# Kernel tuning notes

Measured on AMD Instinct MI355X. Metric: run time of the kernel, lower is better.

## Reference

```python
import jax, jax.numpy as jnp
import numpy as np

D_MODEL = 1024
N_HEAD = 16
D_HEAD = D_MODEL // N_HEAD
B, S = 4, 2048


def setup_inputs() -> dict:
    key = jax.random.key(0)
    ks = jax.random.split(key, 9)
    s = 1.0 / np.sqrt(D_MODEL)
    inp = {"x": jax.random.normal(ks[0], (B, S, D_MODEL), dtype=jnp.float32)}
    for i, name in enumerate(["q", "k", "v", "o"]):
        inp[f"W{name}"] = jax.random.uniform(ks[1 + 2 * i], (D_MODEL, D_MODEL), jnp.float32, -s, s)
        inp[f"b{name}"] = jax.random.uniform(ks[2 + 2 * i], (D_MODEL,), jnp.float32, -s, s)
    return inp


def reference(x, Wq, bq, Wk, bk, Wv, bv, Wo, bo):
    b, sq, _ = x.shape
    skv = sq
    # projections (torch Linear: x @ W^T + b), reshape to (b, h, s, d)
    def proj(W, bias):
        return (x @ W.T + bias).reshape(b, sq, N_HEAD, D_HEAD).transpose(0, 2, 1, 3)
    q, k, v = proj(Wq, bq), proj(Wk, bk), proj(Wv, bv)
    scale = np.sqrt(D_HEAD).astype(np.float32)
    scores = jnp.einsum("bhqd,bhkd->bhqk", q, k) / scale
    causal_mask = jnp.triu(jnp.ones((sq, skv), dtype=bool), k=1)
    scores = jnp.where(causal_mask, -jnp.inf, scores)
    attn = jax.nn.softmax(scores, axis=-1)
    o = jnp.einsum("bhqk,bhkd->bhqd", attn, v)  # (b, h, sq, d_head)
    o = o.transpose(0, 2, 1, 3).reshape(b, sq, D_MODEL)
    return o @ Wo.T + bo
```

## Files before the change

kernel.cpp:

```cpp
#include <hip/hip_runtime.h>
#include <hip/hip_bf16.h>
#include <math.h>

#define S_LEN 2048
#define DMODEL 1024
#define NHEAD 16
#define DHEAD 64
#define BATCH 4
#define MROWS (BATCH * S_LEN)

typedef unsigned short u16;
typedef __attribute__((ext_vector_type(4))) unsigned short u16x4;
typedef __attribute__((ext_vector_type(8))) unsigned short u16x8;
typedef __attribute__((ext_vector_type(2))) unsigned u32x2;
typedef __attribute__((ext_vector_type(4))) unsigned u32x4;
typedef __attribute__((ext_vector_type(8))) short bf16x8;
typedef __attribute__((ext_vector_type(4))) float f32x4;

__device__ __forceinline__ u16 f2bf(float f) {
  unsigned u = __float_as_uint(f);
  u += 0x7fff + ((u >> 16) & 1);
  return (u16)(u >> 16);
}

__device__ __forceinline__ unsigned pkbf2(float lo, float hi) {
  __hip_bfloat162 h = __float22bfloat162_rn(float2{lo, hi});
  unsigned r;
  __builtin_memcpy(&r, &h, 4);
  return r;
}

__device__ __forceinline__ float exp2v(float x) {
  float r;
  asm("v_exp_f32 %0, %1" : "=v"(r) : "v"(x));
  return r;
}

__device__ __forceinline__ f32x4 mfma16(bf16x8 a, bf16x8 b, f32x4 c) {
  return __builtin_amdgcn_mfma_f32_16x16x32_bf16(a, b, c, 0, 0, 0);
}

__global__ __launch_bounds__(256) void castall(
    const float* __restrict__ x,
    const float* __restrict__ w0, const float* __restrict__ w1,
    const float* __restrict__ w2, const float* __restrict__ w3,
    u16* __restrict__ ox,
    u16* __restrict__ o0, u16* __restrict__ o1,
    u16* __restrict__ o2, u16* __restrict__ o3) {
  const int blk = blockIdx.x;
  const float* in;
  u16* out;
  int base;
  if (blk < 4096)      { in = x;  out = ox; base = blk; }
  else if (blk < 4608) { in = w0; out = o0; base = blk - 4096; }
  else if (blk < 5120) { in = w1; out = o1; base = blk - 4608; }
  else if (blk < 5632) { in = w2; out = o2; base = blk - 5120; }
  else                 { in = w3; out = o3; base = blk - 5632; }
  const int i = (base * 256 + threadIdx.x) * 8;
  f32x4 v0 = *(const f32x4*)(in + i);
  f32x4 v1 = *(const f32x4*)(in + i + 4);
  u16x8 o;
#pragma unroll
  for (int j = 0; j < 4; ++j) { o[j] = f2bf(v0[j]); o[4 + j] = f2bf(v1[j]); }
  *(u16x8*)(out + i) = o;
}

__global__ __launch_bounds__(256) void gemm_qkv(
    const u16* __restrict__ Xb,
    const u16* __restrict__ W0, const u16* __restrict__ W1, const u16* __restrict__ W2,
    const float* __restrict__ b0, const float* __restrict__ b1, const float* __restrict__ b2,
    u16* __restrict__ O0, u16* __restrict__ O1, u16* __restrict__ O2) {
  __shared__ u16 As[128 * 64];
  __shared__ u16 Bs[128 * 64];
  const int flat = blockIdx.x;
  const int xcd = flat & 7, idx = flat >> 3;
  const int ymt = xcd * 8 + idx / 24;
  const int rem = idx % 24;
  const int xnt = rem & 7;
  const int z = rem >> 3;
  const u16* Wm = z == 0 ? W0 : (z == 1 ? W1 : W2);
  const float* bias = z == 0 ? b0 : (z == 1 ? b1 : b2);
  u16* Out = z == 0 ? O0 : (z == 1 ? O1 : O2);
  const float qs = (z == 0) ? 0.18033688011112042f : 1.0f;
  const int tid = threadIdx.x;
  const int lane = tid & 63, g = lane >> 4, c = lane & 15;
  const int wave = tid >> 6;
  const int wm = wave >> 1, wn = wave & 1;
  const int bm0 = ymt * 128, bn0 = xnt * 128;

  int srow[4], scol[4];
#pragma unroll
  for (int cc = 0; cc < 4; ++cc) {
    const int ci = cc * 256 + tid;
    srow[cc] = ci >> 3;
    scol[cc] = ((ci & 7) ^ (srow[cc] & 7)) << 3;
  }

  f32x4 acc[4][4];
#pragma unroll
  for (int m = 0; m < 4; ++m)
#pragma unroll
    for (int n = 0; n < 4; ++n) acc[m][n] = (f32x4){0.f, 0.f, 0.f, 0.f};

  u32x4 ar0, ar1, ar2, ar3, br0, br1, br2, br3;
#define GLOAD(k0_) do {                                                        \
    ar0 = *(const u32x4*)(Xb + (size_t)(bm0 + srow[0]) * DMODEL + (k0_) + scol[0]); \
    br0 = *(const u32x4*)(Wm + (size_t)(bn0 + srow[0]) * DMODEL + (k0_) + scol[0]); \
    ar1 = *(const u32x4*)(Xb + (size_t)(bm0 + srow[1]) * DMODEL + (k0_) + scol[1]); \
    br1 = *(const u32x4*)(Wm + (size_t)(bn0 + srow[1]) * DMODEL + (k0_) + scol[1]); \
    ar2 = *(const u32x4*)(Xb + (size_t)(bm0 + srow[2]) * DMODEL + (k0_) + scol[2]); \
    br2 = *(const u32x4*)(Wm + (size_t)(bn0 + srow[2]) * DMODEL + (k0_) + scol[2]); \
    ar3 = *(const u32x4*)(Xb + (size_t)(bm0 + srow[3]) * DMODEL + (k0_) + scol[3]); \
    br3 = *(const u32x4*)(Wm + (size_t)(bn0 + srow[3]) * DMODEL + (k0_) + scol[3]); \
  } while (0)

  GLOAD(0);
  for (int k0 = 0; k0 < DMODEL; k0 += 64) {
    __syncthreads();
    *(u32x4*)((char*)As + (0 * 256 + tid) * 16) = ar0;
    *(u32x4*)((char*)Bs + (0 * 256 + tid) * 16) = br0;
    *(u32x4*)((char*)As + (1 * 256 + tid) * 16) = ar1;
    *(u32x4*)((char*)Bs + (1 * 256 + tid) * 16) = br1;
    *(u32x4*)((char*)As + (2 * 256 + tid) * 16) = ar2;
    *(u32x4*)((char*)Bs + (2 * 256 + tid) * 16) = br2;
    *(u32x4*)((char*)As + (3 * 256 + tid) * 16) = ar3;
    *(u32x4*)((char*)Bs + (3 * 256 + tid) * 16) = br3;
    __syncthreads();
    if (k0 + 64 < DMODEL) GLOAD(k0 + 64);
#pragma unroll
    for (int ks = 0; ks < 2; ++ks) {
      bf16x8 af[4], bfr[4];
#pragma unroll
      for (int m = 0; m < 4; ++m) {
        const int arow = wm * 64 + m * 16 + c;
        af[m] = *(const bf16x8*)((const char*)As + arow * 128 +
                                 (((ks * 4 + g) ^ (arow & 7)) << 4));
      }
#pragma unroll
      for (int n = 0; n < 4; ++n) {
        const int brow = wn * 64 + n * 16 + c;
        bfr[n] = *(const bf16x8*)((const char*)Bs + brow * 128 +
                                  (((ks * 4 + g) ^ (brow & 7)) << 4));
      }
#pragma unroll
      for (int m = 0; m < 4; ++m)
#pragma unroll
        for (int n = 0; n < 4; ++n)
          acc[m][n] = mfma16(af[m], bfr[n], acc[m][n]);
    }
  }
#undef GLOAD
  if (z < 2) {
#pragma unroll
    for (int n = 0; n < 4; ++n) {
      const int coln = bn0 + wn * 64 + n * 16 + c;
      const float bn_ = bias[coln];
      const int h = coln >> 6, d = coln & 63;
#pragma unroll
      for (int m = 0; m < 4; ++m) {
#pragma unroll
        for (int r = 0; r < 4; ++r) {
          const int rowm = bm0 + wm * 64 + m * 16 + g * 4 + r;
          const int b_ = rowm >> 11, s_ = rowm & 2047;
          Out[(((size_t)(b_ * NHEAD + h) * S_LEN + s_) << 6) + d] =
              f2bf((acc[m][n][r] + bn_) * qs);
        }
      }
    }
  } else {
#pragma unroll
    for (int n = 0; n < 4; ++n) {
      const int coln = bn0 + wn * 64 + n * 16 + c;
      const float bn_ = bias[coln];
      const int h = coln >> 6, d = coln & 63;
#pragma unroll
      for (int m = 0; m < 4; ++m) {
        const int row0 = bm0 + wm * 64 + m * 16 + g * 4;
        const int b_ = row0 >> 11, s_ = row0 & 2047;
        u16x4 pk;
#pragma unroll
        for (int r = 0; r < 4; ++r) pk[r] = f2bf(acc[m][n][r] + bn_);
        *(u16x4*)(Out + ((size_t)(b_ * NHEAD + h) * DHEAD + d) * S_LEN + s_) = pk;
      }
    }
  }
}

__global__ __launch_bounds__(256) void gemm_out(
    const u16* __restrict__ Ab, const u16* __restrict__ Wm,
    const float* __restrict__ bias, float* __restrict__ Out) {
  __shared__ u16 As[128 * 64];
  __shared__ u16 Bs[128 * 64];
  const int flat = blockIdx.x;
  const int xcd = flat & 7, idx = flat >> 3;
  const int ymt = xcd * 8 + (idx >> 3);
  const int xnt = idx & 7;
  const int tid = threadIdx.x;
  const int lane = tid & 63, g = lane >> 4, c = lane & 15;
  const int wave = tid >> 6;
  const int wm = wave >> 1, wn = wave & 1;
  const int bm0 = ymt * 128, bn0 = xnt * 128;

  int srow[4], scol[4];
#pragma unroll
  for (int cc = 0; cc < 4; ++cc) {
    const int ci = cc * 256 + tid;
    srow[cc] = ci >> 3;
    scol[cc] = ((ci & 7) ^ (srow[cc] & 7)) << 3;
  }

  f32x4 acc[4][4];
#pragma unroll
  for (int m = 0; m < 4; ++m)
#pragma unroll
    for (int n = 0; n < 4; ++n) acc[m][n] = (f32x4){0.f, 0.f, 0.f, 0.f};

  u32x4 ar0, ar1, ar2, ar3, br0, br1, br2, br3;
#define GLOAD(k0_) do {                                                        \
    ar0 = *(const u32x4*)(Ab + (size_t)(bm0 + srow[0]) * DMODEL + (k0_) + scol[0]); \
    br0 = *(const u32x4*)(Wm + (size_t)(bn0 + srow[0]) * DMODEL + (k0_) + scol[0]); \
    ar1 = *(const u32x4*)(Ab + (size_t)(bm0 + srow[1]) * DMODEL + (k0_) + scol[1]); \
    br1 = *(const u32x4*)(Wm + (size_t)(bn0 + srow[1]) * DMODEL + (k0_) + scol[1]); \
    ar2 = *(const u32x4*)(Ab + (size_t)(bm0 + srow[2]) * DMODEL + (k0_) + scol[2]); \
    br2 = *(const u32x4*)(Wm + (size_t)(bn0 + srow[2]) * DMODEL + (k0_) + scol[2]); \
    ar3 = *(const u32x4*)(Ab + (size_t)(bm0 + srow[3]) * DMODEL + (k0_) + scol[3]); \
    br3 = *(const u32x4*)(Wm + (size_t)(bn0 + srow[3]) * DMODEL + (k0_) + scol[3]); \
  } while (0)

  GLOAD(0);
  for (int k0 = 0; k0 < DMODEL; k0 += 64) {
    __syncthreads();
    *(u32x4*)((char*)As + (0 * 256 + tid) * 16) = ar0;
    *(u32x4*)((char*)Bs + (0 * 256 + tid) * 16) = br0;
    *(u32x4*)((char*)As + (1 * 256 + tid) * 16) = ar1;
    *(u32x4*)((char*)Bs + (1 * 256 + tid) * 16) = br1;
    *(u32x4*)((char*)As + (2 * 256 + tid) * 16) = ar2;
    *(u32x4*)((char*)Bs + (2 * 256 + tid) * 16) = br2;
    *(u32x4*)((char*)As + (3 * 256 + tid) * 16) = ar3;
    *(u32x4*)((char*)Bs + (3 * 256 + tid) * 16) = br3;
    __syncthreads();
    if (k0 + 64 < DMODEL) GLOAD(k0 + 64);
#pragma unroll
    for (int ks = 0; ks < 2; ++ks) {
      bf16x8 af[4], bfr[4];
#pragma unroll
      for (int m = 0; m < 4; ++m) {
        const int arow = wm * 64 + m * 16 + c;
        af[m] = *(const bf16x8*)((const char*)As + arow * 128 +
                                 (((ks * 4 + g) ^ (arow & 7)) << 4));
      }
#pragma unroll
      for (int n = 0; n < 4; ++n) {
        const int brow = wn * 64 + n * 16 + c;
        bfr[n] = *(const bf16x8*)((const char*)Bs + brow * 128 +
                                  (((ks * 4 + g) ^ (brow & 7)) << 4));
      }
#pragma unroll
      for (int m = 0; m < 4; ++m)
#pragma unroll
        for (int n = 0; n < 4; ++n)
          acc[m][n] = mfma16(af[m], bfr[n], acc[m][n]);
    }
  }
#undef GLOAD
#pragma unroll
  for (int n = 0; n < 4; ++n) {
    const int coln = bn0 + wn * 64 + n * 16 + c;
    const float bn_ = bias[coln];
#pragma unroll
    for (int m = 0; m < 4; ++m) {
#pragma unroll
      for (int r = 0; r < 4; ++r) {
        const int rowm = bm0 + wm * 64 + m * 16 + g * 4 + r;
        Out[(size_t)rowm * DMODEL + coln] = acc[m][n][r] + bn_;
      }
    }
  }
}

__global__ __launch_bounds__(256) void attn_fwd(const u16* __restrict__ Qb,
                                                const u16* __restrict__ Kb,
                                                const u16* __restrict__ VTb,
                                                u16* __restrict__ AOb) {
  __shared__ u16 Kt[64 * 64];
  __shared__ u16 Vt[64 * 64];
  __shared__ unsigned Pl[4][16 * 36];
  const int tid = threadIdx.x;
  const int w = tid >> 6, lane = tid & 63, g = lane >> 4, c = lane & 15;
  const int flat = blockIdx.x;
  const int xcd = flat & 7, idx = flat >> 3;
  const int qt = 31 - (idx >> 3);
  const int bh = xcd * 8 + (idx & 7);
  const size_t base = (size_t)bh * (S_LEN * DHEAD);
  const int b_ = bh >> 4, h = bh & 15;
  const int ci0 = w * 64 + lane;

  const int row0_ = ci0 >> 3,            colg0 = (ci0 & 7) ^ (row0_ & 7);
  const int row1_ = (256 + ci0) >> 3,    colg1 = ((256 + ci0) & 7) ^ (row1_ & 7);

  const int qb = qt * 64;
  const int q = qb + w * 16 + c;
  const bf16x8 qf0 = *(const bf16x8*)(Qb + base + (size_t)q * 64 + g * 8);
  const bf16x8 qf1 = *(const bf16x8*)(Qb + base + (size_t)q * 64 + 32 + g * 8);

  f32x4 oacc[4];
#pragma unroll
  for (int dt = 0; dt < 4; ++dt) oacc[dt] = (f32x4){0.f, 0.f, 0.f, 0.f};
  float m = -30000.f, l = 0.f;

  u32x4 kreg0, kreg1, vreg0, vreg1;
#define STAGE_LOAD(kt_) do {                                                  \
    const int kv0_ = (kt_) * 64;                                              \
    kreg0 = *(const u32x4*)(Kb + base + (size_t)(kv0_ + row0_) * 64 + colg0 * 8); \
    vreg0 = *(const u32x4*)(VTb + base + (size_t)row0_ * S_LEN + kv0_ + colg0 * 8); \
    kreg1 = *(const u32x4*)(Kb + base + (size_t)(kv0_ + row1_) * 64 + colg1 * 8); \
    vreg1 = *(const u32x4*)(VTb + base + (size_t)row1_ * S_LEN + kv0_ + colg1 * 8); \
  } while (0)

  const int nt = qt + 1;
  STAGE_LOAD(0);
  for (int kt = 0; kt < nt; ++kt) {
    const int kv0 = kt * 64;
    __syncthreads();
    *(u32x4*)((char*)Kt + ci0 * 16) = kreg0;
    *(u32x4*)((char*)Vt + ci0 * 16) = vreg0;
    *(u32x4*)((char*)Kt + (256 + ci0) * 16) = kreg1;
    *(u32x4*)((char*)Vt + (256 + ci0) * 16) = vreg1;
    __syncthreads();
    if (kt + 1 < nt) STAGE_LOAD(kt + 1);

    f32x4 s[4];
#pragma unroll
    for (int t = 0; t < 4; ++t) {
      const int krow = t * 16 + c;
      const char* kbase = (const char*)Kt + krow * 128;
      bf16x8 kf0 = *(const bf16x8*)(kbase + ((g ^ (krow & 7)) * 16));
      bf16x8 kf1 = *(const bf16x8*)(kbase + (((4 + g) ^ (krow & 7)) * 16));
      f32x4 zacc = (f32x4){0.f, 0.f, 0.f, 0.f};
      zacc = mfma16(kf0, qf0, zacc);
      zacc = mfma16(kf1, qf1, zacc);
      s[t] = zacc;
    }
    if (kt == nt - 1) {
#pragma unroll
      for (int t = 0; t < 4; ++t)
#pragma unroll
        for (int r = 0; r < 4; ++r)
          if (kv0 + t * 16 + 4 * g + r > q) s[t][r] = -30000.f;
    }
    const float a0 = fmaxf(fmaxf(s[0][0], s[0][1]), s[0][2]);
    const float a1 = fmaxf(fmaxf(s[0][3], s[1][0]), s[1][1]);
    const float a2 = fmaxf(fmaxf(s[1][2], s[1][3]), s[2][0]);
    const float a3 = fmaxf(fmaxf(s[2][1], s[2][2]), s[2][3]);
    const float a4 = fmaxf(fmaxf(s[3][0], s[3][1]), s[3][2]);
    float pm = fmaxf(fmaxf(fmaxf(a0, a1), a2), fmaxf(fmaxf(a3, a4), s[3][3]));
    pm = fmaxf(pm, __shfl_xor(pm, 16));
    pm = fmaxf(pm, __shfl_xor(pm, 32));
    if (__any(pm > m + 8.0f)) {
      const float mn = fmaxf(m, pm);
      const float sc = exp2v(m - mn);
      l *= sc;
#pragma unroll
      for (int dt = 0; dt < 4; ++dt) oacc[dt] *= sc;
      m = mn;
    }
    float rs = 0.f;
#pragma unroll
    for (int t = 0; t < 4; ++t) {
      const float p0 = exp2v(s[t][0] - m), p1 = exp2v(s[t][1] - m);
      const float p2 = exp2v(s[t][2] - m), p3 = exp2v(s[t][3] - m);
      rs += (p0 + p1) + (p2 + p3);
      u32x2 pk2;
      pk2[0] = pkbf2(p0, p1);
      pk2[1] = pkbf2(p2, p3);
      *(u32x2*)&Pl[w][c * 36 + t * 8 + g * 2] = pk2;
    }
    rs += __shfl_xor(rs, 16);
    rs += __shfl_xor(rs, 32);
    l += rs;

#pragma unroll
    for (int kk = 0; kk < 2; ++kk) {
      const bf16x8 pb = *(const bf16x8*)&Pl[w][c * 36 + kk * 16 + g * 4];
#pragma unroll
      for (int dt = 0; dt < 4; ++dt) {
        const int vrow = dt * 16 + c;
        const bf16x8 vf = *(const bf16x8*)((const char*)Vt + vrow * 128 +
                                           (((kk * 4 + g) ^ (vrow & 7)) * 16));
        oacc[dt] = mfma16(vf, pb, oacc[dt]);
      }
    }
  }
#undef STAGE_LOAD
  const float inv = 1.0f / l;
  const size_t rowbase = ((size_t)(b_ * S_LEN + q) * DMODEL) + h * 64;
#pragma unroll
  for (int dt = 0; dt < 4; ++dt) {
    u16x4 pk4;
#pragma unroll
    for (int r = 0; r < 4; ++r) pk4[r] = f2bf(oacc[dt][r] * inv);
    *(u16x4*)(AOb + rowbase + dt * 16 + 4 * g) = pk4;
  }
}

extern "C" void kernel_launch(void* const* d_in, const int* in_sizes, int n_in,
                              void* d_out, int out_size, void* d_ws, size_t ws_size,
                              hipStream_t stream) {
  const float* x  = (const float*)d_in[0];
  const float* Wq = (const float*)d_in[1];
  const float* bq = (const float*)d_in[2];
  const float* Wk = (const float*)d_in[3];
  const float* bk = (const float*)d_in[4];
  const float* Wv = (const float*)d_in[5];
  const float* bv = (const float*)d_in[6];
  const float* Wo = (const float*)d_in[7];
  const float* bo = (const float*)d_in[8];
  float* out = (float*)d_out;
  char* ws = (char*)d_ws;

  const size_t MB = 1024 * 1024;
  u16* xb  = (u16*)(ws);
  u16* Wqb = (u16*)(ws + 16 * MB);
  u16* Wkb = (u16*)(ws + 18 * MB);
  u16* Wvb = (u16*)(ws + 20 * MB);
  u16* Wob = (u16*)(ws + 22 * MB);
  u16* Qb  = (u16*)(ws + 24 * MB);
  u16* Kb  = (u16*)(ws + 40 * MB);
  u16* VTb = (u16*)(ws + 56 * MB);
  u16* AOb = (u16*)(ws + 72 * MB);

  castall<<<6144, 256, 0, stream>>>(x, Wq, Wk, Wv, Wo, xb, Wqb, Wkb, Wvb, Wob);

  gemm_qkv<<<1536, 256, 0, stream>>>(
      xb, Wqb, Wkb, Wvb, bq, bk, bv, Qb, Kb, VTb);

  attn_fwd<<<2048, 256, 0, stream>>>(Qb, Kb, VTb, AOb);

  gemm_out<<<512, 256, 0, stream>>>(AOb, Wob, bo, out);
}
```

Before: 171.5 us.

## Fuse x bf16 cast into QKV GEMM loads and compute softmax row-sum via MFMA

Removes the separate cast pass over x: the QKV GEMM now loads fp32 x directly and converts it to bf16 while staging into LDS, and the cast kernel only handles the weights. This avoids writing and re-reading a 16MB bf16 copy of x, at the cost of the GEMM reading twice the bytes for A, once per column tile. Separately, attention now accumulates the softmax denominator with an extra MFMA against a ones vector instead of scalar adds and cross-lane shuffles. The row sum is therefore built from bf16-rounded probabilities, matching what multiplies V.

```diff
diff --git a/kernel.cpp b/kernel.cpp
--- a/kernel.cpp
+++ b/kernel.cpp
@@ -41,21 +41,14 @@
 }
 
 __global__ __launch_bounds__(256) void castall(
-    const float* __restrict__ x,
     const float* __restrict__ w0, const float* __restrict__ w1,
     const float* __restrict__ w2, const float* __restrict__ w3,
-    u16* __restrict__ ox,
     u16* __restrict__ o0, u16* __restrict__ o1,
     u16* __restrict__ o2, u16* __restrict__ o3) {
   const int blk = blockIdx.x;
-  const float* in;
-  u16* out;
-  int base;
-  if (blk < 4096)      { in = x;  out = ox; base = blk; }
-  else if (blk < 4608) { in = w0; out = o0; base = blk - 4096; }
-  else if (blk < 5120) { in = w1; out = o1; base = blk - 4608; }
-  else if (blk < 5632) { in = w2; out = o2; base = blk - 5120; }
-  else                 { in = w3; out = o3; base = blk - 5632; }
+  const int mtx = blk >> 9, base = blk & 511;
+  const float* in = mtx == 0 ? w0 : (mtx == 1 ? w1 : (mtx == 2 ? w2 : w3));
+  u16* out = mtx == 0 ? o0 : (mtx == 1 ? o1 : (mtx == 2 ? o2 : o3));
   const int i = (base * 256 + threadIdx.x) * 8;
   f32x4 v0 = *(const f32x4*)(in + i);
   f32x4 v1 = *(const f32x4*)(in + i + 4);
@@ -66,7 +59,7 @@
 }
 
 __global__ __launch_bounds__(256) void gemm_qkv(
-    const u16* __restrict__ Xb,
+    const float* __restrict__ Xf,
     const u16* __restrict__ W0, const u16* __restrict__ W1, const u16* __restrict__ W2,
     const float* __restrict__ b0, const float* __restrict__ b1, const float* __restrict__ b2,
     u16* __restrict__ O0, u16* __restrict__ O1, u16* __restrict__ O2) {
@@ -102,29 +95,31 @@
 #pragma unroll
     for (int n = 0; n < 4; ++n) acc[m][n] = (f32x4){0.f, 0.f, 0.f, 0.f};
 
-  u32x4 ar0, ar1, ar2, ar3, br0, br1, br2, br3;
+  f32x4 axl[4], axh[4];
+  u32x4 brx[4];
 #define GLOAD(k0_) do {                                                        \
-    ar0 = *(const u32x4*)(Xb + (size_t)(bm0 + srow[0]) * DMODEL + (k0_) + scol[0]); \
-    br0 = *(const u32x4*)(Wm + (size_t)(bn0 + srow[0]) * DMODEL + (k0_) + scol[0]); \
-    ar1 = *(const u32x4*)(Xb + (size_t)(bm0 + srow[1]) * DMODEL + (k0_) + scol[1]); \
-    br1 = *(const u32x4*)(Wm + (size_t)(bn0 + srow[1]) * DMODEL + (k0_) + scol[1]); \
-    ar2 = *(const u32x4*)(Xb + (size_t)(bm0 + srow[2]) * DMODEL + (k0_) + scol[2]); \
-    br2 = *(const u32x4*)(Wm + (size_t)(bn0 + srow[2]) * DMODEL + (k0_) + scol[2]); \
-    ar3 = *(const u32x4*)(Xb + (size_t)(bm0 + srow[3]) * DMODEL + (k0_) + scol[3]); \
-    br3 = *(const u32x4*)(Wm + (size_t)(bn0 + srow[3]) * DMODEL + (k0_) + scol[3]); \
+    _Pragma("unroll")                                                          \
+    for (int cc = 0; cc < 4; ++cc) {                                           \
+      const float* xp = Xf + (size_t)(bm0 + srow[cc]) * DMODEL + (k0_) + scol[cc]; \
+      axl[cc] = *(const f32x4*)xp;                                             \
+      axh[cc] = *(const f32x4*)(xp + 4);                                       \
+      brx[cc] = *(const u32x4*)(Wm + (size_t)(bn0 + srow[cc]) * DMODEL + (k0_) + scol[cc]); \
+    }                                                                          \
   } while (0)
 
   GLOAD(0);
   for (int k0 = 0; k0 < DMODEL; k0 += 64) {
     __syncthreads();
-    *(u32x4*)((char*)As + (0 * 256 + tid) * 16) = ar0;
-    *(u32x4*)((char*)Bs + (0 * 256 + tid) * 16) = br0;
-    *(u32x4*)((char*)As + (1 * 256 + tid) * 16) = ar1;
-    *(u32x4*)((char*)Bs + (1 * 256 + tid) * 16) = br1;
-    *(u32x4*)((char*)As + (2 * 256 + tid) * 16) = ar2;
-    *(u32x4*)((char*)Bs + (2 * 256 + tid) * 16) = br2;
-    *(u32x4*)((char*)As + (3 * 256 + tid) * 16) = ar3;
-    *(u32x4*)((char*)Bs + (3 * 256 + tid) * 16) = br3;
+#pragma unroll
+    for (int cc = 0; cc < 4; ++cc) {
+      u32x4 aw;
+      aw[0] = pkbf2(axl[cc][0], axl[cc][1]);
+      aw[1] = pkbf2(axl[cc][2], axl[cc][3]);
+      aw[2] = pkbf2(axh[cc][0], axh[cc][1]);
+      aw[3] = pkbf2(axh[cc][2], axh[cc][3]);
+      *(u32x4*)((char*)As + (cc * 256 + tid) * 16) = aw;
+      *(u32x4*)((char*)Bs + (cc * 256 + tid) * 16) = brx[cc];
+    }
     __syncthreads();
     if (k0 + 64 < DMODEL) GLOAD(k0 + 64);
 #pragma unroll
@@ -303,10 +298,15 @@
   const bf16x8 qf0 = *(const bf16x8*)(Qb + base + (size_t)q * 64 + g * 8);
   const bf16x8 qf1 = *(const bf16x8*)(Qb + base + (size_t)q * 64 + 32 + g * 8);
 
+  bf16x8 ones;
+#pragma unroll
+  for (int j = 0; j < 8; ++j) ones[j] = (short)0x3F80;
+
   f32x4 oacc[4];
+  f32x4 lacc = (f32x4){0.f, 0.f, 0.f, 0.f};
 #pragma unroll
   for (int dt = 0; dt < 4; ++dt) oacc[dt] = (f32x4){0.f, 0.f, 0.f, 0.f};
-  float m = -30000.f, l = 0.f;
+  float m = -30000.f;
 
   u32x4 kreg0, kreg1, vreg0, vreg1;
 #define STAGE_LOAD(kt_) do {                                                  \
@@ -359,29 +359,25 @@
     if (__any(pm > m + 8.0f)) {
       const float mn = fmaxf(m, pm);
       const float sc = exp2v(m - mn);
-      l *= sc;
+      lacc *= sc;
 #pragma unroll
       for (int dt = 0; dt < 4; ++dt) oacc[dt] *= sc;
       m = mn;
     }
-    float rs = 0.f;
 #pragma unroll
     for (int t = 0; t < 4; ++t) {
       const float p0 = exp2v(s[t][0] - m), p1 = exp2v(s[t][1] - m);
       const float p2 = exp2v(s[t][2] - m), p3 = exp2v(s[t][3] - m);
-      rs += (p0 + p1) + (p2 + p3);
       u32x2 pk2;
       pk2[0] = pkbf2(p0, p1);
       pk2[1] = pkbf2(p2, p3);
       *(u32x2*)&Pl[w][c * 36 + t * 8 + g * 2] = pk2;
     }
-    rs += __shfl_xor(rs, 16);
-    rs += __shfl_xor(rs, 32);
-    l += rs;
 
 #pragma unroll
     for (int kk = 0; kk < 2; ++kk) {
       const bf16x8 pb = *(const bf16x8*)&Pl[w][c * 36 + kk * 16 + g * 4];
+      lacc = mfma16(ones, pb, lacc);
 #pragma unroll
       for (int dt = 0; dt < 4; ++dt) {
         const int vrow = dt * 16 + c;
@@ -392,7 +388,7 @@
     }
   }
 #undef STAGE_LOAD
-  const float inv = 1.0f / l;
+  const float inv = 1.0f / lacc[0];
   const size_t rowbase = ((size_t)(b_ * S_LEN + q) * DMODEL) + h * 64;
 #pragma unroll
   for (int dt = 0; dt < 4; ++dt) {
@@ -419,7 +415,6 @@
   char* ws = (char*)d_ws;
 
   const size_t MB = 1024 * 1024;
-  u16* xb  = (u16*)(ws);
   u16* Wqb = (u16*)(ws + 16 * MB);
   u16* Wkb = (u16*)(ws + 18 * MB);
   u16* Wvb = (u16*)(ws + 20 * MB);
@@ -429,10 +424,10 @@
   u16* VTb = (u16*)(ws + 56 * MB);
   u16* AOb = (u16*)(ws + 72 * MB);
 
-  castall<<<6144, 256, 0, stream>>>(x, Wq, Wk, Wv, Wo, xb, Wqb, Wkb, Wvb, Wob);
+  castall<<<2048, 256, 0, stream>>>(Wq, Wk, Wv, Wo, Wqb, Wkb, Wvb, Wob);
 
   gemm_qkv<<<1536, 256, 0, stream>>>(
-      xb, Wqb, Wkb, Wvb, bq, bk, bv, Qb, Kb, VTb);
+      x, Wqb, Wkb, Wvb, bq, bk, bv, Qb, Kb, VTb);
 
   attn_fwd<<<2048, 256, 0, stream>>>(Qb, Kb, VTb, AOb);
 
```

Result: slower. 175.6 us (+2.4%).
